# Kernel tuning notes

Hardware: AMD Instinct MI355X
Metric: run time of the kernel (lower is better)

## Reference

```python
import jax, jax.numpy as jnp
import numpy as np

B, H, S, D = 4, 16, 2048, 128


def setup_inputs() -> dict:
    key = jax.random.key(0)
    kq, kk, kv, km = jax.random.split(key, 4)
    query = jax.random.normal(kq, (B, H, S, D), dtype=jnp.float32)
    k = jax.random.normal(kk, (B, H, S, D), dtype=jnp.float32)
    value = jax.random.normal(kv, (B, H, S, D), dtype=jnp.float32)
    mask = jax.random.randint(km, (B, 1, S, S), 0, 2, dtype=jnp.int32)
    return {"query": query, "key": k, "value": value, "mask": mask, "softmax_dim": -1}


def reference(query, key, value, mask, softmax_dim):
    dk = query.shape[-1]
    # scores: [B, H, S, S]
    scores = jnp.einsum("bhqd,bhkd->bhqk", query, key) / jnp.sqrt(jnp.float32(dk))
    scores = jnp.where(mask == 0, jnp.float32(-1e9), scores)
    attention = jax.nn.softmax(scores, axis=softmax_dim)
    out = jnp.einsum("bhqk,bhkd->bhqd", attention, value)
    return (out, attention)
```

## Files before the change

### kernel.cpp

```cpp
#include <hip/hip_runtime.h>

typedef __attribute__((ext_vector_type(8))) short short8;
typedef __attribute__((ext_vector_type(4))) short short4v;
typedef __attribute__((ext_vector_type(4))) float float4v;

#define B_ 4
#define H_ 16
#define S_ 2048
#define D_ 128
#define BM 64
#define NKT64 32
#define NKT32 64

#define NSH (B_ * H_ * S_ * D_)
#define NMW ((size_t)B_ * 32 * S_)
#define WS_NEED (2ull * (unsigned long long)NSH * 2ull + (unsigned long long)NMW * 8ull)

#define QSCALE (0.08838834764831845f * 1.4426950408889634f)

__device__ __forceinline__ unsigned cvtpk(float lo, float hi) {
  unsigned r;
  asm("v_cvt_pk_bf16_f32 %0, %1, %2" : "=v"(r) : "v"(lo), "v"(hi));
  return r;
}

__device__ __forceinline__ short f2bf(float f) {
  unsigned u = __float_as_uint(f);
  u = (u + 0x7fffu + ((u >> 16) & 1u)) >> 16;
  return (short)u;
}

__device__ __forceinline__ void gl16(const void* g, void* lds) {
  __builtin_amdgcn_global_load_lds(
      (const __attribute__((address_space(1))) unsigned int*)g,
      (__attribute__((address_space(3))) unsigned int*)lds, 16, 0, 0);
}

__global__ void prep_kv(const float* __restrict__ Kg, const float* __restrict__ Vg,
                        short* __restrict__ Kf, short* __restrict__ Vf, int half) {
  size_t id = (size_t)blockIdx.x * 256 + threadIdx.x;
  if (blockIdx.x < (unsigned)half) {
    int c  = (int)(id & 15);
    int g  = (int)((id >> 4) & 3);
    int dc = (int)((id >> 6) & 3);
    int kf = (int)((id >> 8) & 3);
    int kt = (int)((id >> 10) & 31);
    size_t bh = id >> 15;
    const float* src = Kg + ((bh * S_ + (size_t)(kt * 64 + kf * 16 + c)) * D_) + dc * 32 + g * 8;
    float4v a = *(const float4v*)src;
    float4v b = *(const float4v*)(src + 4);
    int4 s;
    s.x = (int)cvtpk(a[0], a[1]);
    s.y = (int)cvtpk(a[2], a[3]);
    s.z = (int)cvtpk(b[0], b[1]);
    s.w = (int)cvtpk(b[2], b[3]);
    ((int4*)Kf)[id] = s;
  } else {
    id -= (size_t)half * 256;
    int c   = (int)(id & 15);
    int g   = (int)((id >> 4) & 3);
    int df  = (int)((id >> 6) & 7);
    int kt32= (int)((id >> 9) & 63);
    size_t bh = id >> 15;
    const float* src = Vg + (bh * S_ + (size_t)(kt32 * 32 + g * 8)) * D_ + df * 16 + c;
    float f[8];
#pragma unroll
    for (int e = 0; e < 8; ++e) f[e] = src[(size_t)e * D_];
    int4 s;
    s.x = (int)cvtpk(f[0], f[1]);
    s.y = (int)cvtpk(f[2], f[3]);
    s.z = (int)cvtpk(f[4], f[5]);
    s.w = (int)cvtpk(f[6], f[7]);
    ((int4*)Vf)[id] = s;
  }
}

__global__ void prep_m(const int* __restrict__ Mg, unsigned long long* __restrict__ Bits) {
  int gw = blockIdx.x * 4 + (threadIdx.x >> 6);
  int j  = threadIdx.x & 63;
  int kt = gw & 31;
  int q  = (gw >> 5) & (S_ - 1);
  int b  = gw >> 16;
  int m = Mg[((size_t)b * S_ + q) * S_ + kt * 64 + j];
  unsigned long long bal = __ballot(m != 0);
  if (j == 0) Bits[((size_t)b * 32 + kt) * S_ + q] = bal;
}

__global__ __launch_bounds__(256, 4) void sdpa_main(
    const float* __restrict__ Qg, const short* __restrict__ Kfr,
    const short* __restrict__ Vfr, const unsigned long long* __restrict__ Bits,
    float* __restrict__ Og, float* __restrict__ Ag) {

  __shared__ __align__(16) char smem[32768 + 5120];
  short (*Ps)[40] = (short (*)[40])(smem + 32768);

  const int t = threadIdx.x;
  const int w = t >> 6;
  const int l = t & 63;
  const int g = l >> 4;

  const int p    = blockIdx.x;
  const int xcd  = p & 7;
  const int slot = p >> 3;
  const int grp  = ((slot >> 5) << 3) + xcd;
  const int qt   = slot & 31;
  const int h    = grp & 15;
  const int b    = grp >> 4;

  const int qbase  = qt * BM;
  const int qrow_l = w * 16 + (l & 15);
  const int qrow   = qbase + qrow_l;

  const size_t bhOff = (size_t)(b * H_ + h) * (S_ * D_);
  const short* Kp = Kfr + bhOff;
  const short* Vp = Vfr + bhOff;
  const unsigned long long* Bp = Bits + (size_t)b * 32 * S_;
  const unsigned* Bu = (const unsigned*)Bits;
  float* Op = Og + bhOff;
  float* Ap = Ag + (size_t)(b * H_ + h) * ((size_t)S_ * S_);

  short8 qf[4];
#pragma unroll
  for (int dc = 0; dc < 4; ++dc) {
    const float* qsrc = Qg + bhOff + (size_t)qrow * D_ + dc * 32 + g * 8;
    float4v a = *(const float4v*)qsrc;
    float4v c4 = *(const float4v*)(qsrc + 4);
    int4 s;
    s.x = (int)cvtpk(a[0] * QSCALE, a[1] * QSCALE);
    s.y = (int)cvtpk(a[2] * QSCALE, a[3] * QSCALE);
    s.z = (int)cvtpk(c4[0] * QSCALE, c4[1] * QSCALE);
    s.w = (int)cvtpk(c4[2] * QSCALE, c4[3] * QSCALE);
    qf[dc] = *(short8*)&s;
  }

#pragma unroll
  for (int i = 0; i < 4; ++i) {
    int f = w * 4 + i;
    gl16(Kp + f * 512 + l * 8, smem + f * 1024);
  }
  __syncthreads();

  float ls0 = 0.f, ls1 = 0.f, ls2 = 0.f, ls3 = 0.f;
  unsigned long long mb = Bp[qrow];
  int cur = 0;
  for (int kt = 0; kt < NKT64; ++kt) {
    unsigned long long mb_next = 0;
    if (kt < NKT64 - 1) {
      mb_next = Bp[(size_t)(kt + 1) * S_ + qrow];
      const short* src = Kp + (size_t)(kt + 1) * 8192;
      char* dst = smem + (cur ^ 1) * 16384;
#pragma unroll
      for (int i = 0; i < 4; ++i) {
        int f = w * 4 + i;
        gl16(src + f * 512 + l * 8, dst + f * 1024);
      }
    }
    const char* kb = smem + cur * 16384;

    float4v acc[4];
#pragma unroll
    for (int kf = 0; kf < 4; ++kf) acc[kf] = (float4v){0.f, 0.f, 0.f, 0.f};
#pragma unroll
    for (int kf = 0; kf < 4; ++kf) {
#pragma unroll
      for (int dc = 0; dc < 4; ++dc) {
        short8 af = *(const short8*)(kb + (kf * 4 + dc) * 1024 + l * 16);
        acc[kf] = __builtin_amdgcn_mfma_f32_16x16x32_bf16(af, qf[dc], acc[kf], 0, 0, 0);
      }
    }
#pragma unroll
    for (int kf = 0; kf < 4; ++kf) {
      unsigned mg = (unsigned)(mb >> (kf * 16 + g * 4)) & 0xFu;
      float p0 = ((mg >> 0) & 1) ? __builtin_amdgcn_exp2f(acc[kf][0]) : 0.f;
      float p1 = ((mg >> 1) & 1) ? __builtin_amdgcn_exp2f(acc[kf][1]) : 0.f;
      float p2 = ((mg >> 2) & 1) ? __builtin_amdgcn_exp2f(acc[kf][2]) : 0.f;
      float p3 = ((mg >> 3) & 1) ? __builtin_amdgcn_exp2f(acc[kf][3]) : 0.f;
      if (kf == 0) ls0 += (p0 + p1) + (p2 + p3);
      else if (kf == 1) ls1 += (p0 + p1) + (p2 + p3);
      else if (kf == 2) ls2 += (p0 + p1) + (p2 + p3);
      else ls3 += (p0 + p1) + (p2 + p3);
    }
    __syncthreads();
    mb = mb_next;
    cur ^= 1;
  }
  float lsum = (ls0 + ls1) + (ls2 + ls3);
  lsum += __shfl_xor(lsum, 16);
  lsum += __shfl_xor(lsum, 32);
  const float lg = (lsum > 0.f) ? __log2f(lsum) : 1e30f;

#pragma unroll
  for (int i = 0; i < 2; ++i) {
    int f = w + 4 * i;
    gl16(Kp + f * 512 + l * 8, smem + f * 1024);
    gl16(Vp + f * 512 + l * 8, smem + 16384 + f * 1024);
  }
  __syncthreads();

  float4v acco[8];
#pragma unroll
  for (int df = 0; df < 8; ++df) acco[df] = (float4v){0.f, 0.f, 0.f, 0.f};

  unsigned mw = Bu[((size_t)(b * 32) * S_ + qrow) * 2];
  cur = 0;
  for (int kt = 0; kt < NKT32; ++kt) {
    unsigned mw_next = 0;
    if (kt < NKT32 - 1) {
      mw_next = Bu[((size_t)(b * 32 + ((kt + 1) >> 1)) * S_ + qrow) * 2 + ((kt + 1) & 1)];
      const short* ks = Kp + (size_t)(kt + 1) * 4096;
      const short* vs = Vp + (size_t)(kt + 1) * 4096;
      char* kd = smem + (cur ^ 1) * 8192;
      char* vd = smem + 16384 + (cur ^ 1) * 8192;
#pragma unroll
      for (int i = 0; i < 2; ++i) {
        int f = w + 4 * i;
        gl16(ks + f * 512 + l * 8, kd + f * 1024);
        gl16(vs + f * 512 + l * 8, vd + f * 1024);
      }
    }
    const char* kb = smem + cur * 8192;
    const char* vb = smem + 16384 + cur * 8192;

    float4v acc[2];
#pragma unroll
    for (int kf = 0; kf < 2; ++kf) acc[kf] = (float4v){0.f, 0.f, 0.f, 0.f};
#pragma unroll
    for (int kf = 0; kf < 2; ++kf) {
#pragma unroll
      for (int dc = 0; dc < 4; ++dc) {
        short8 af = *(const short8*)(kb + (kf * 4 + dc) * 1024 + l * 16);
        acc[kf] = __builtin_amdgcn_mfma_f32_16x16x32_bf16(af, qf[dc], acc[kf], 0, 0, 0);
      }
    }

    float4v aw[2];
#pragma unroll
    for (int kf = 0; kf < 2; ++kf) {
      unsigned mg = (mw >> (kf * 16 + g * 4)) & 0xFu;
#pragma unroll
      for (int r = 0; r < 4; ++r) {
        float arg = ((mg >> r) & 1) ? (acc[kf][r] - lg) : -1e30f;
        aw[kf][r] = __builtin_amdgcn_exp2f(arg);
      }
      int2 pb;
      pb.x = (int)cvtpk(aw[kf][0], aw[kf][1]);
      pb.y = (int)cvtpk(aw[kf][2], aw[kf][3]);
      *(int2*)&Ps[qrow_l][kf * 16 + g * 4] = pb;
    }

    {
      short8 pbf = *(const short8*)&Ps[qrow_l][g * 8];
#pragma unroll
      for (int df = 0; df < 8; ++df) {
        short8 vf = *(const short8*)(vb + df * 1024 + l * 16);
        acco[df] = __builtin_amdgcn_mfma_f32_16x16x32_bf16(vf, pbf, acco[df], 0, 0, 0);
      }
    }
#pragma unroll
    for (int kf = 0; kf < 2; ++kf) {
      int k0 = kt * 32 + kf * 16 + g * 4;
      __builtin_nontemporal_store(aw[kf], (float4v*)(Ap + (size_t)qrow * S_ + k0));
    }
    __syncthreads();
    mw = mw_next;
    cur ^= 1;
  }

#pragma unroll
  for (int df = 0; df < 8; ++df) {
    __builtin_nontemporal_store(acco[df], (float4v*)(Op + (size_t)qrow * D_ + df * 16 + g * 4));
  }
}

#define LQK 136
#define LVT 72

__global__ __launch_bounds__(256, 3) void sdpa_fallback(
    const float* __restrict__ Qg, const float* __restrict__ Kg,
    const float* __restrict__ Vg, const int* __restrict__ Mg,
    float* __restrict__ Og, float* __restrict__ Ag) {

  __shared__ __align__(16) char smemf[17408 + 27648];
  short (*Ks)[LQK]  = (short (*)[LQK])(smemf);
  short (*Qs)[LQK]  = (short (*)[LQK])(smemf + 17408);
  short (*VTs)[LVT] = (short (*)[LVT])(smemf + 17408);
  short (*Psf)[LVT] = (short (*)[LVT])(smemf + 17408 + 18432);

  const int t = threadIdx.x;
  const int w = t >> 6;
  const int l = t & 63;
  const int g = l >> 4;
  const int c = l & 15;

  const int bid = blockIdx.x;
  const int qt = bid & 31;
  const int h  = (bid >> 5) & 15;
  const int b  = bid >> 9;

  const int qbase  = qt * BM;
  const int qrow_l = w * 16 + c;
  const int qrow   = qbase + qrow_l;

  const size_t bhOff = (size_t)(b * H_ + h) * (S_ * D_);
  const float* Qp = Qg + bhOff;
  const float* Kp = Kg + bhOff;
  const float* Vp = Vg + bhOff;
  const int*   Mp = Mg + (size_t)b * S_ * S_;
  float* Op = Og + bhOff;
  float* Ap = Ag + (size_t)(b * H_ + h) * ((size_t)S_ * S_);

#pragma unroll
  for (int i = 0; i < 8; ++i) {
    int idx = t + i * 256;
    int d4 = idx & 31, row = idx >> 5;
    float4v v = *(const float4v*)(Qp + (size_t)(qbase + row) * D_ + d4 * 4);
    short4v s;
    s[0] = f2bf(v[0] * QSCALE); s[1] = f2bf(v[1] * QSCALE);
    s[2] = f2bf(v[2] * QSCALE); s[3] = f2bf(v[3] * QSCALE);
    *(short4v*)&Qs[row][d4 * 4] = s;
  }
  __syncthreads();

  short8 qf[4];
#pragma unroll
  for (int dc = 0; dc < 4; ++dc)
    qf[dc] = *(const short8*)&Qs[qrow_l][dc * 32 + g * 8];

  float m_run = -1e30f, l_run = 0.f;
  for (int kt = 0; kt < 32; ++kt) {
    __syncthreads();
#pragma unroll
    for (int i = 0; i < 8; ++i) {
      int idx = t + i * 256;
      int d4 = idx & 31, row = idx >> 5;
      float4v v = *(const float4v*)(Kp + (size_t)(kt * 64 + row) * D_ + d4 * 4);
      short4v s;
      s[0] = f2bf(v[0]); s[1] = f2bf(v[1]); s[2] = f2bf(v[2]); s[3] = f2bf(v[3]);
      *(short4v*)&Ks[row][d4 * 4] = s;
    }
    __syncthreads();

    float4v acc[4];
#pragma unroll
    for (int kf = 0; kf < 4; ++kf) acc[kf] = (float4v){0.f, 0.f, 0.f, 0.f};
#pragma unroll
    for (int kf = 0; kf < 4; ++kf) {
#pragma unroll
      for (int dc = 0; dc < 4; ++dc) {
        short8 af = *(const short8*)&Ks[kf * 16 + c][dc * 32 + g * 8];
        acc[kf] = __builtin_amdgcn_mfma_f32_16x16x32_bf16(af, qf[dc], acc[kf], 0, 0, 0);
      }
    }

    float sv[4][4];
    float tmax = -1e30f;
#pragma unroll
    for (int kf = 0; kf < 4; ++kf) {
      int k0 = kt * 64 + kf * 16 + g * 4;
      const int4 mv = *(const int4*)(Mp + (size_t)qrow * S_ + k0);
      int mr[4] = {mv.x, mv.y, mv.z, mv.w};
#pragma unroll
      for (int r = 0; r < 4; ++r) {
        float x = acc[kf][r];
        x = (mr[r] == 0) ? -1e9f : x;
        sv[kf][r] = x;
        tmax = fmaxf(tmax, x);
      }
    }
    tmax = fmaxf(tmax, __shfl_xor(tmax, 16));
    tmax = fmaxf(tmax, __shfl_xor(tmax, 32));
    float newm = fmaxf(m_run, tmax);
    float tsum = 0.f;
#pragma unroll
    for (int kf = 0; kf < 4; ++kf)
#pragma unroll
      for (int r = 0; r < 4; ++r)
        tsum += __builtin_amdgcn_exp2f(sv[kf][r] - newm);
    tsum += __shfl_xor(tsum, 16);
    tsum += __shfl_xor(tsum, 32);
    l_run = l_run * __builtin_amdgcn_exp2f(m_run - newm) + tsum;
    m_run = newm;
  }

  const float rl = 1.0f / l_run;

  float4v acco[8];
#pragma unroll
  for (int df = 0; df < 8; ++df) acco[df] = (float4v){0.f, 0.f, 0.f, 0.f};

  for (int kt = 0; kt < 32; ++kt) {
    __syncthreads();
#pragma unroll
    for (int i = 0; i < 8; ++i) {
      int idx = t + i * 256;
      int d4 = idx & 31, row = idx >> 5;
      float4v v = *(const float4v*)(Kp + (size_t)(kt * 64 + row) * D_ + d4 * 4);
      short4v s;
      s[0] = f2bf(v[0]); s[1] = f2bf(v[1]); s[2] = f2bf(v[2]); s[3] = f2bf(v[3]);
      *(short4v*)&Ks[row][d4 * 4] = s;
    }
#pragma unroll
    for (int i = 0; i < 8; ++i) {
      int idx = t + i * 256;
      int d = idx & 127, kq = idx >> 7;
      const float* vp = Vp + (size_t)(kt * 64 + kq * 4) * D_ + d;
      short4v s;
      s[0] = f2bf(vp[0]); s[1] = f2bf(vp[D_]); s[2] = f2bf(vp[2 * D_]); s[3] = f2bf(vp[3 * D_]);
      *(short4v*)&VTs[d][kq * 4] = s;
    }
    __syncthreads();

    float4v acc[4];
#pragma unroll
    for (int kf = 0; kf < 4; ++kf) acc[kf] = (float4v){0.f, 0.f, 0.f, 0.f};
#pragma unroll
    for (int kf = 0; kf < 4; ++kf) {
#pragma unroll
      for (int dc = 0; dc < 4; ++dc) {
        short8 af = *(const short8*)&Ks[kf * 16 + c][dc * 32 + g * 8];
        acc[kf] = __builtin_amdgcn_mfma_f32_16x16x32_bf16(af, qf[dc], acc[kf], 0, 0, 0);
      }
    }

#pragma unroll
    for (int kf = 0; kf < 4; ++kf) {
      int k0 = kt * 64 + kf * 16 + g * 4;
      const int4 mv = *(const int4*)(Mp + (size_t)qrow * S_ + k0);
      int mr[4] = {mv.x, mv.y, mv.z, mv.w};
      float4v aw;
      short4v pb;
#pragma unroll
      for (int r = 0; r < 4; ++r) {
        float x = acc[kf][r];
        x = (mr[r] == 0) ? -1e9f : x;
        float pn = __builtin_amdgcn_exp2f(x - m_run) * rl;
        aw[r] = pn;
        pb[r] = f2bf(pn);
      }
      __builtin_nontemporal_store(aw, (float4v*)(Ap + (size_t)qrow * S_ + k0));
      *(short4v*)&Psf[qrow_l][kf * 16 + g * 4] = pb;
    }

#pragma unroll
    for (int kc = 0; kc < 2; ++kc) {
      short8 pbf = *(const short8*)&Psf[qrow_l][kc * 32 + g * 8];
#pragma unroll
      for (int df = 0; df < 8; ++df) {
        short8 vf = *(const short8*)&VTs[df * 16 + c][kc * 32 + g * 8];
        acco[df] = __builtin_amdgcn_mfma_f32_16x16x32_bf16(vf, pbf, acco[df], 0, 0, 0);
      }
    }
  }

#pragma unroll
  for (int df = 0; df < 8; ++df) {
    *(float4v*)(Op + (size_t)qrow * D_ + df * 16 + g * 4) = acco[df];
  }
}

extern "C" void kernel_launch(void* const* d_in, const int* in_sizes, int n_in,
                              void* d_out, int out_size, void* d_ws, size_t ws_size,
                              hipStream_t stream) {
  const float* Q = (const float*)d_in[0];
  const float* K = (const float*)d_in[1];
  const float* V = (const float*)d_in[2];
  const int*   M = (const int*)d_in[3];
  float* Out  = (float*)d_out;
  float* Attn = Out + (size_t)B_ * H_ * S_ * D_;

  if (ws_size >= WS_NEED) {
    short* Kf = (short*)d_ws;
    short* Vf = Kf + (size_t)NSH;
    unsigned long long* Bits = (unsigned long long*)(Vf + (size_t)NSH);
    const int pgrid = NSH / 8 / 256;
    prep_kv<<<dim3(pgrid * 2), dim3(256), 0, stream>>>(K, V, Kf, Vf, pgrid);
    prep_m<<<dim3((unsigned)(NMW / 4)), dim3(256), 0, stream>>>(M, Bits);
    sdpa_main<<<dim3(B_ * H_ * (S_ / BM)), dim3(256), 0, stream>>>(
        Q, Kf, Vf, Bits, Out, Attn);
  } else {
    sdpa_fallback<<<dim3(B_ * H_ * (S_ / BM)), dim3(256), 0, stream>>>(Q, K, V, M, Out, Attn);
  }
}
```

Before: 432.5 us.

## Prefetch K/V tiles two iterations ahead with explicit vmcnt waits

Both main loops now keep two tiles in flight instead of one. They issue loads for tile kt+2 into the freed buffer after the compute barrier, and gate each iteration with hand-counted s_waitcnt vmcnt values plus a raw s_barrier in place of __syncthreads. The aim is to hide global-to-LDS latency and avoid draining all outstanding memory operations, including the attention nontemporal stores, at every barrier. The risk is that the hand-counted vmcnt values are fragile: if the compiler reorders or adds memory operations, a wait may be too loose and read stale LDS.

```diff
diff --git a/kernel.cpp b/kernel.cpp
--- a/kernel.cpp
+++ b/kernel.cpp
@@ -17,6 +17,12 @@
 #define WS_NEED (2ull * (unsigned long long)NSH * 2ull + (unsigned long long)NMW * 8ull)
 
 #define QSCALE (0.08838834764831845f * 1.4426950408889634f)
+
+#define WAITV0() asm volatile("s_waitcnt vmcnt(0)" ::: "memory")
+#define WAITV2() asm volatile("s_waitcnt vmcnt(2)" ::: "memory")
+#define WAITV5() asm volatile("s_waitcnt vmcnt(5)" ::: "memory")
+#define WAITV7() asm volatile("s_waitcnt vmcnt(7)" ::: "memory")
+#define BARR()   asm volatile("s_barrier" ::: "memory")
 
 __device__ __forceinline__ unsigned cvtpk(float lo, float hi) {
   unsigned r;
@@ -138,24 +144,19 @@
     int f = w * 4 + i;
     gl16(Kp + f * 512 + l * 8, smem + f * 1024);
   }
-  __syncthreads();
+  unsigned long long mb0 = Bp[qrow];
+#pragma unroll
+  for (int i = 0; i < 4; ++i) {
+    int f = w * 4 + i;
+    gl16(Kp + 8192 + f * 512 + l * 8, smem + 16384 + f * 1024);
+  }
+  unsigned long long mb1 = Bp[(size_t)S_ + qrow];
 
   float ls0 = 0.f, ls1 = 0.f, ls2 = 0.f, ls3 = 0.f;
-  unsigned long long mb = Bp[qrow];
-  int cur = 0;
   for (int kt = 0; kt < NKT64; ++kt) {
-    unsigned long long mb_next = 0;
-    if (kt < NKT64 - 1) {
-      mb_next = Bp[(size_t)(kt + 1) * S_ + qrow];
-      const short* src = Kp + (size_t)(kt + 1) * 8192;
-      char* dst = smem + (cur ^ 1) * 16384;
-#pragma unroll
-      for (int i = 0; i < 4; ++i) {
-        int f = w * 4 + i;
-        gl16(src + f * 512 + l * 8, dst + f * 1024);
-      }
-    }
-    const char* kb = smem + cur * 16384;
+    if (kt < NKT64 - 1) { WAITV5(); } else { WAITV0(); }
+    BARR();
+    const char* kb = smem + (kt & 1) * 16384;
 
     float4v acc[4];
 #pragma unroll
@@ -170,7 +171,7 @@
     }
 #pragma unroll
     for (int kf = 0; kf < 4; ++kf) {
-      unsigned mg = (unsigned)(mb >> (kf * 16 + g * 4)) & 0xFu;
+      unsigned mg = (unsigned)(mb0 >> (kf * 16 + g * 4)) & 0xFu;
       float p0 = ((mg >> 0) & 1) ? __builtin_amdgcn_exp2f(acc[kf][0]) : 0.f;
       float p1 = ((mg >> 1) & 1) ? __builtin_amdgcn_exp2f(acc[kf][1]) : 0.f;
       float p2 = ((mg >> 2) & 1) ? __builtin_amdgcn_exp2f(acc[kf][2]) : 0.f;
@@ -180,9 +181,19 @@
       else if (kf == 2) ls2 += (p0 + p1) + (p2 + p3);
       else ls3 += (p0 + p1) + (p2 + p3);
     }
-    __syncthreads();
-    mb = mb_next;
-    cur ^= 1;
+    BARR();
+    unsigned long long mb2 = 0;
+    if (kt < NKT64 - 2) {
+      const short* src = Kp + (size_t)(kt + 2) * 8192;
+      char* dst = smem + (kt & 1) * 16384;
+#pragma unroll
+      for (int i = 0; i < 4; ++i) {
+        int f = w * 4 + i;
+        gl16(src + f * 512 + l * 8, dst + f * 1024);
+      }
+      mb2 = Bp[(size_t)(kt + 2) * S_ + qrow];
+    }
+    mb0 = mb1; mb1 = mb2;
   }
   float lsum = (ls0 + ls1) + (ls2 + ls3);
   lsum += __shfl_xor(lsum, 16);
@@ -195,75 +206,83 @@
     gl16(Kp + f * 512 + l * 8, smem + f * 1024);
     gl16(Vp + f * 512 + l * 8, smem + 16384 + f * 1024);
   }
-  __syncthreads();
+  unsigned mw0 = Bu[((size_t)(b * 32) * S_ + qrow) * 2];
+#pragma unroll
+  for (int i = 0; i < 2; ++i) {
+    int f = w + 4 * i;
+    gl16(Kp + 4096 + f * 512 + l * 8, smem + 8192 + f * 1024);
+    gl16(Vp + 4096 + f * 512 + l * 8, smem + 16384 + 8192 + f * 1024);
+  }
+  unsigned mw1 = Bu[((size_t)(b * 32) * S_ + qrow) * 2 + 1];
 
   float4v acco[8];
 #pragma unroll
   for (int df = 0; df < 8; ++df) acco[df] = (float4v){0.f, 0.f, 0.f, 0.f};
 
-  unsigned mw = Bu[((size_t)(b * 32) * S_ + qrow) * 2];
-  cur = 0;
   for (int kt = 0; kt < NKT32; ++kt) {
-    unsigned mw_next = 0;
-    if (kt < NKT32 - 1) {
-      mw_next = Bu[((size_t)(b * 32 + ((kt + 1) >> 1)) * S_ + qrow) * 2 + ((kt + 1) & 1)];
-      const short* ks = Kp + (size_t)(kt + 1) * 4096;
-      const short* vs = Vp + (size_t)(kt + 1) * 4096;
-      char* kd = smem + (cur ^ 1) * 8192;
-      char* vd = smem + 16384 + (cur ^ 1) * 8192;
+    if (kt == 0) { WAITV5(); }
+    else if (kt < NKT32 - 1) { WAITV7(); }
+    else { WAITV2(); }
+    BARR();
+    const char* kb = smem + (kt & 1) * 8192;
+    const char* vb = smem + 16384 + (kt & 1) * 8192;
+
+    float4v acc[2];
+#pragma unroll
+    for (int kf = 0; kf < 2; ++kf) acc[kf] = (float4v){0.f, 0.f, 0.f, 0.f};
+#pragma unroll
+    for (int kf = 0; kf < 2; ++kf) {
+#pragma unroll
+      for (int dc = 0; dc < 4; ++dc) {
+        short8 af = *(const short8*)(kb + (kf * 4 + dc) * 1024 + l * 16);
+        acc[kf] = __builtin_amdgcn_mfma_f32_16x16x32_bf16(af, qf[dc], acc[kf], 0, 0, 0);
+      }
+    }
+
+    float4v aw[2];
+#pragma unroll
+    for (int kf = 0; kf < 2; ++kf) {
+      unsigned mg = (mw0 >> (kf * 16 + g * 4)) & 0xFu;
+#pragma unroll
+      for (int r = 0; r < 4; ++r) {
+        float arg = ((mg >> r) & 1) ? (acc[kf][r] - lg) : -1e30f;
+        aw[kf][r] = __builtin_amdgcn_exp2f(arg);
+      }
+      int2 pb;
+      pb.x = (int)cvtpk(aw[kf][0], aw[kf][1]);
+      pb.y = (int)cvtpk(aw[kf][2], aw[kf][3]);
+      *(int2*)&Ps[qrow_l][kf * 16 + g * 4] = pb;
+    }
+
+    {
+      short8 pbf = *(const short8*)&Ps[qrow_l][g * 8];
+#pragma unroll
+      for (int df = 0; df < 8; ++df) {
+        short8 vf = *(const short8*)(vb + df * 1024 + l * 16);
+        acco[df] = __builtin_amdgcn_mfma_f32_16x16x32_bf16(vf, pbf, acco[df], 0, 0, 0);
+      }
+    }
+    BARR();
+    unsigned mw2 = 0;
+    if (kt < NKT32 - 2) {
+      const short* ks = Kp + (size_t)(kt + 2) * 4096;
+      const short* vs = Vp + (size_t)(kt + 2) * 4096;
+      char* kd = smem + (kt & 1) * 8192;
+      char* vd = smem + 16384 + (kt & 1) * 8192;
 #pragma unroll
       for (int i = 0; i < 2; ++i) {
         int f = w + 4 * i;
         gl16(ks + f * 512 + l * 8, kd + f * 1024);
         gl16(vs + f * 512 + l * 8, vd + f * 1024);
       }
-    }
-    const char* kb = smem + cur * 8192;
-    const char* vb = smem + 16384 + cur * 8192;
-
-    float4v acc[2];
-#pragma unroll
-    for (int kf = 0; kf < 2; ++kf) acc[kf] = (float4v){0.f, 0.f, 0.f, 0.f};
-#pragma unroll
-    for (int kf = 0; kf < 2; ++kf) {
-#pragma unroll
-      for (int dc = 0; dc < 4; ++dc) {
-        short8 af = *(const short8*)(kb + (kf * 4 + dc) * 1024 + l * 16);
-        acc[kf] = __builtin_amdgcn_mfma_f32_16x16x32_bf16(af, qf[dc], acc[kf], 0, 0, 0);
-      }
-    }
-
-    float4v aw[2];
-#pragma unroll
-    for (int kf = 0; kf < 2; ++kf) {
-      unsigned mg = (mw >> (kf * 16 + g * 4)) & 0xFu;
-#pragma unroll
-      for (int r = 0; r < 4; ++r) {
-        float arg = ((mg >> r) & 1) ? (acc[kf][r] - lg) : -1e30f;
-        aw[kf][r] = __builtin_amdgcn_exp2f(arg);
-      }
-      int2 pb;
-      pb.x = (int)cvtpk(aw[kf][0], aw[kf][1]);
-      pb.y = (int)cvtpk(aw[kf][2], aw[kf][3]);
-      *(int2*)&Ps[qrow_l][kf * 16 + g * 4] = pb;
-    }
-
-    {
-      short8 pbf = *(const short8*)&Ps[qrow_l][g * 8];
-#pragma unroll
-      for (int df = 0; df < 8; ++df) {
-        short8 vf = *(const short8*)(vb + df * 1024 + l * 16);
-        acco[df] = __builtin_amdgcn_mfma_f32_16x16x32_bf16(vf, pbf, acco[df], 0, 0, 0);
-      }
+      mw2 = Bu[((size_t)(b * 32 + ((kt + 2) >> 1)) * S_ + qrow) * 2 + ((kt + 2) & 1)];
     }
 #pragma unroll
     for (int kf = 0; kf < 2; ++kf) {
       int k0 = kt * 32 + kf * 16 + g * 4;
       __builtin_nontemporal_store(aw[kf], (float4v*)(Ap + (size_t)qrow * S_ + k0));
     }
-    __syncthreads();
-    mw = mw_next;
-    cur ^= 1;
+    mw0 = mw1; mw1 = mw2;
   }
 
 #pragma unroll
```

New measurement: 437.8 us. No clear change (+1.2%).

## Double query tile per block so each wave reuses K/V fragments across two row groups

Applied to the files above, without the earlier changes.

Raises the query tile from 64 to 128 rows, with each wave handling two 16-row groups that share every K and V fragment loaded from LDS. This halves K/V global and LDS traffic per query row and halves the block count. In exchange it doubles accumulator registers, lowers the occupancy hint from 4 to 3 blocks, grows shared memory for P, and leaves fewer blocks to fill the GPU. The fallback kernel is pinned to the old 64-row tiling.

```diff
diff --git a/kernel.cpp b/kernel.cpp
--- a/kernel.cpp
+++ b/kernel.cpp
@@ -8,7 +8,7 @@
 #define H_ 16
 #define S_ 2048
 #define D_ 128
-#define BM 64
+#define BM 128
 #define NKT64 32
 #define NKT32 64
 
@@ -86,12 +86,12 @@
   if (j == 0) Bits[((size_t)b * 32 + kt) * S_ + q] = bal;
 }
 
-__global__ __launch_bounds__(256, 4) void sdpa_main(
+__global__ __launch_bounds__(256, 3) void sdpa_main(
     const float* __restrict__ Qg, const short* __restrict__ Kfr,
     const short* __restrict__ Vfr, const unsigned long long* __restrict__ Bits,
     float* __restrict__ Og, float* __restrict__ Ag) {
 
-  __shared__ __align__(16) char smem[32768 + 5120];
+  __shared__ __align__(16) char smem[32768 + 10240];
   short (*Ps)[40] = (short (*)[40])(smem + 32768);
 
   const int t = threadIdx.x;
@@ -102,14 +102,15 @@
   const int p    = blockIdx.x;
   const int xcd  = p & 7;
   const int slot = p >> 3;
-  const int grp  = ((slot >> 5) << 3) + xcd;
-  const int qt   = slot & 31;
+  const int grp  = ((slot >> 4) << 3) + xcd;
+  const int qt   = slot & 15;
   const int h    = grp & 15;
   const int b    = grp >> 4;
 
   const int qbase  = qt * BM;
-  const int qrow_l = w * 16 + (l & 15);
-  const int qrow   = qbase + qrow_l;
+  const int r0     = w * 32 + (l & 15);
+  const int qrow0  = qbase + r0;
+  const int qrow1  = qrow0 + 16;
 
   const size_t bhOff = (size_t)(b * H_ + h) * (S_ * D_);
   const short* Kp = Kfr + bhOff;
@@ -119,18 +120,26 @@
   float* Op = Og + bhOff;
   float* Ap = Ag + (size_t)(b * H_ + h) * ((size_t)S_ * S_);
 
-  short8 qf[4];
+  short8 qf0[4], qf1[4];
 #pragma unroll
   for (int dc = 0; dc < 4; ++dc) {
-    const float* qsrc = Qg + bhOff + (size_t)qrow * D_ + dc * 32 + g * 8;
-    float4v a = *(const float4v*)qsrc;
-    float4v c4 = *(const float4v*)(qsrc + 4);
+    const float* q0 = Qg + bhOff + (size_t)qrow0 * D_ + dc * 32 + g * 8;
+    float4v a = *(const float4v*)q0;
+    float4v c4 = *(const float4v*)(q0 + 4);
     int4 s;
     s.x = (int)cvtpk(a[0] * QSCALE, a[1] * QSCALE);
     s.y = (int)cvtpk(a[2] * QSCALE, a[3] * QSCALE);
     s.z = (int)cvtpk(c4[0] * QSCALE, c4[1] * QSCALE);
     s.w = (int)cvtpk(c4[2] * QSCALE, c4[3] * QSCALE);
-    qf[dc] = *(short8*)&s;
+    qf0[dc] = *(short8*)&s;
+    const float* q1 = Qg + bhOff + (size_t)qrow1 * D_ + dc * 32 + g * 8;
+    a = *(const float4v*)q1;
+    c4 = *(const float4v*)(q1 + 4);
+    s.x = (int)cvtpk(a[0] * QSCALE, a[1] * QSCALE);
+    s.y = (int)cvtpk(a[2] * QSCALE, a[3] * QSCALE);
+    s.z = (int)cvtpk(c4[0] * QSCALE, c4[1] * QSCALE);
+    s.w = (int)cvtpk(c4[2] * QSCALE, c4[3] * QSCALE);
+    qf1[dc] = *(short8*)&s;
   }
 
 #pragma unroll
@@ -140,13 +149,14 @@
   }
   __syncthreads();
 
-  float ls0 = 0.f, ls1 = 0.f, ls2 = 0.f, ls3 = 0.f;
-  unsigned long long mb = Bp[qrow];
+  float lsA0 = 0.f, lsA1 = 0.f, lsB0 = 0.f, lsB1 = 0.f;
+  unsigned long long mbA = Bp[qrow0], mbB = Bp[qrow1];
   int cur = 0;
   for (int kt = 0; kt < NKT64; ++kt) {
-    unsigned long long mb_next = 0;
+    unsigned long long mbA2 = 0, mbB2 = 0;
     if (kt < NKT64 - 1) {
-      mb_next = Bp[(size_t)(kt + 1) * S_ + qrow];
+      mbA2 = Bp[(size_t)(kt + 1) * S_ + qrow0];
+      mbB2 = Bp[(size_t)(kt + 1) * S_ + qrow1];
       const short* src = Kp + (size_t)(kt + 1) * 8192;
       char* dst = smem + (cur ^ 1) * 16384;
 #pragma unroll
@@ -157,37 +167,45 @@
     }
     const char* kb = smem + cur * 16384;
 
-    float4v acc[4];
-#pragma unroll
-    for (int kf = 0; kf < 4; ++kf) acc[kf] = (float4v){0.f, 0.f, 0.f, 0.f};
+    float4v accA[4], accB[4];
+#pragma unroll
+    for (int kf = 0; kf < 4; ++kf) { accA[kf] = (float4v){0.f,0.f,0.f,0.f}; accB[kf] = (float4v){0.f,0.f,0.f,0.f}; }
 #pragma unroll
     for (int kf = 0; kf < 4; ++kf) {
 #pragma unroll
       for (int dc = 0; dc < 4; ++dc) {
         short8 af = *(const short8*)(kb + (kf * 4 + dc) * 1024 + l * 16);
-        acc[kf] = __builtin_amdgcn_mfma_f32_16x16x32_bf16(af, qf[dc], acc[kf], 0, 0, 0);
+        accA[kf] = __builtin_amdgcn_mfma_f32_16x16x32_bf16(af, qf0[dc], accA[kf], 0, 0, 0);
+        accB[kf] = __builtin_amdgcn_mfma_f32_16x16x32_bf16(af, qf1[dc], accB[kf], 0, 0, 0);
       }
     }
 #pragma unroll
     for (int kf = 0; kf < 4; ++kf) {
-      unsigned mg = (unsigned)(mb >> (kf * 16 + g * 4)) & 0xFu;
-      float p0 = ((mg >> 0) & 1) ? __builtin_amdgcn_exp2f(acc[kf][0]) : 0.f;
-      float p1 = ((mg >> 1) & 1) ? __builtin_amdgcn_exp2f(acc[kf][1]) : 0.f;
-      float p2 = ((mg >> 2) & 1) ? __builtin_amdgcn_exp2f(acc[kf][2]) : 0.f;
-      float p3 = ((mg >> 3) & 1) ? __builtin_amdgcn_exp2f(acc[kf][3]) : 0.f;
-      if (kf == 0) ls0 += (p0 + p1) + (p2 + p3);
-      else if (kf == 1) ls1 += (p0 + p1) + (p2 + p3);
-      else if (kf == 2) ls2 += (p0 + p1) + (p2 + p3);
-      else ls3 += (p0 + p1) + (p2 + p3);
+      unsigned mgA = (unsigned)(mbA >> (kf * 16 + g * 4)) & 0xFu;
+      float a0 = ((mgA >> 0) & 1) ? __builtin_amdgcn_exp2f(accA[kf][0]) : 0.f;
+      float a1 = ((mgA >> 1) & 1) ? __builtin_amdgcn_exp2f(accA[kf][1]) : 0.f;
+      float a2 = ((mgA >> 2) & 1) ? __builtin_amdgcn_exp2f(accA[kf][2]) : 0.f;
+      float a3 = ((mgA >> 3) & 1) ? __builtin_amdgcn_exp2f(accA[kf][3]) : 0.f;
+      if (kf & 1) lsA1 += (a0 + a1) + (a2 + a3); else lsA0 += (a0 + a1) + (a2 + a3);
+      unsigned mgB = (unsigned)(mbB >> (kf * 16 + g * 4)) & 0xFu;
+      float b0 = ((mgB >> 0) & 1) ? __builtin_amdgcn_exp2f(accB[kf][0]) : 0.f;
+      float b1 = ((mgB >> 1) & 1) ? __builtin_amdgcn_exp2f(accB[kf][1]) : 0.f;
+      float b2 = ((mgB >> 2) & 1) ? __builtin_amdgcn_exp2f(accB[kf][2]) : 0.f;
+      float b3 = ((mgB >> 3) & 1) ? __builtin_amdgcn_exp2f(accB[kf][3]) : 0.f;
+      if (kf & 1) lsB1 += (b0 + b1) + (b2 + b3); else lsB0 += (b0 + b1) + (b2 + b3);
     }
     __syncthreads();
-    mb = mb_next;
+    mbA = mbA2; mbB = mbB2;
     cur ^= 1;
   }
-  float lsum = (ls0 + ls1) + (ls2 + ls3);
-  lsum += __shfl_xor(lsum, 16);
-  lsum += __shfl_xor(lsum, 32);
-  const float lg = (lsum > 0.f) ? __log2f(lsum) : 1e30f;
+  float lsumA = lsA0 + lsA1;
+  lsumA += __shfl_xor(lsumA, 16);
+  lsumA += __shfl_xor(lsumA, 32);
+  const float lgA = (lsumA > 0.f) ? __log2f(lsumA) : 1e30f;
+  float lsumB = lsB0 + lsB1;
+  lsumB += __shfl_xor(lsumB, 16);
+  lsumB += __shfl_xor(lsumB, 32);
+  const float lgB = (lsumB > 0.f) ? __log2f(lsumB) : 1e30f;
 
 #pragma unroll
   for (int i = 0; i < 2; ++i) {
@@ -197,16 +215,18 @@
   }
   __syncthreads();
 
-  float4v acco[8];
-#pragma unroll
-  for (int df = 0; df < 8; ++df) acco[df] = (float4v){0.f, 0.f, 0.f, 0.f};
-
-  unsigned mw = Bu[((size_t)(b * 32) * S_ + qrow) * 2];
+  float4v accoA[8], accoB[8];
+#pragma unroll
+  for (int df = 0; df < 8; ++df) { accoA[df] = (float4v){0.f,0.f,0.f,0.f}; accoB[df] = (float4v){0.f,0.f,0.f,0.f}; }
+
+  unsigned mwA = Bu[((size_t)(b * 32) * S_ + qrow0) * 2];
+  unsigned mwB = Bu[((size_t)(b * 32) * S_ + qrow1) * 2];
   cur = 0;
   for (int kt = 0; kt < NKT32; ++kt) {
-    unsigned mw_next = 0;
+    unsigned mwA2 = 0, mwB2 = 0;
     if (kt < NKT32 - 1) {
-      mw_next = Bu[((size_t)(b * 32 + ((kt + 1) >> 1)) * S_ + qrow) * 2 + ((kt + 1) & 1)];
+      mwA2 = Bu[((size_t)(b * 32 + ((kt + 1) >> 1)) * S_ + qrow0) * 2 + ((kt + 1) & 1)];
+      mwB2 = Bu[((size_t)(b * 32 + ((kt + 1) >> 1)) * S_ + qrow1) * 2 + ((kt + 1) & 1)];
       const short* ks = Kp + (size_t)(kt + 1) * 4096;
       const short* vs = Vp + (size_t)(kt + 1) * 4096;
       char* kd = smem + (cur ^ 1) * 8192;
@@ -221,54 +241,68 @@
     const char* kb = smem + cur * 8192;
     const char* vb = smem + 16384 + cur * 8192;
 
-    float4v acc[2];
-#pragma unroll
-    for (int kf = 0; kf < 2; ++kf) acc[kf] = (float4v){0.f, 0.f, 0.f, 0.f};
+    float4v accA[2], accB[2];
+#pragma unroll
+    for (int kf = 0; kf < 2; ++kf) { accA[kf] = (float4v){0.f,0.f,0.f,0.f}; accB[kf] = (float4v){0.f,0.f,0.f,0.f}; }
 #pragma unroll
     for (int kf = 0; kf < 2; ++kf) {
 #pragma unroll
       for (int dc = 0; dc < 4; ++dc) {
         short8 af = *(const short8*)(kb + (kf * 4 + dc) * 1024 + l * 16);
-        acc[kf] = __builtin_amdgcn_mfma_f32_16x16x32_bf16(af, qf[dc], acc[kf], 0, 0, 0);
-      }
-    }
-
-    float4v aw[2];
+        accA[kf] = __builtin_amdgcn_mfma_f32_16x16x32_bf16(af, qf0[dc], accA[kf], 0, 0, 0);
+        accB[kf] = __builtin_amdgcn_mfma_f32_16x16x32_bf16(af, qf1[dc], accB[kf], 0, 0, 0);
+      }
+    }
+
+    float4v awA[2], awB[2];
 #pragma unroll
     for (int kf = 0; kf < 2; ++kf) {
-      unsigned mg = (mw >> (kf * 16 + g * 4)) & 0xFu;
+      unsigned mgA = (mwA >> (kf * 16 + g * 4)) & 0xFu;
 #pragma unroll
       for (int r = 0; r < 4; ++r) {
-        float arg = ((mg >> r) & 1) ? (acc[kf][r] - lg) : -1e30f;
-        aw[kf][r] = __builtin_amdgcn_exp2f(arg);
+        float arg = ((mgA >> r) & 1) ? (accA[kf][r] - lgA) : -1e30f;
+        awA[kf][r] = __builtin_amdgcn_exp2f(arg);
       }
       int2 pb;
-      pb.x = (int)cvtpk(aw[kf][0], aw[kf][1]);
-      pb.y = (int)cvtpk(aw[kf][2], aw[kf][3]);
-      *(int2*)&Ps[qrow_l][kf * 16 + g * 4] = pb;
+      pb.x = (int)cvtpk(awA[kf][0], awA[kf][1]);
+      pb.y = (int)cvtpk(awA[kf][2], awA[kf][3]);
+      *(int2*)&Ps[r0][kf * 16 + g * 4] = pb;
+      unsigned mgB = (mwB >> (kf * 16 + g * 4)) & 0xFu;
+#pragma unroll
+      for (int r = 0; r < 4; ++r) {
+        float arg = ((mgB >> r) & 1) ? (accB[kf][r] - lgB) : -1e30f;
+        awB[kf][r] = __builtin_amdgcn_exp2f(arg);
+      }
+      pb.x = (int)cvtpk(awB[kf][0], awB[kf][1]);
+      pb.y = (int)cvtpk(awB[kf][2], awB[kf][3]);
+      *(int2*)&Ps[r0 + 16][kf * 16 + g * 4] = pb;
     }
 
     {
-      short8 pbf = *(const short8*)&Ps[qrow_l][g * 8];
+      short8 pbfA = *(const short8*)&Ps[r0][g * 8];
+      short8 pbfB = *(const short8*)&Ps[r0 + 16][g * 8];
 #pragma unroll
       for (int df = 0; df < 8; ++df) {
         short8 vf = *(const short8*)(vb + df * 1024 + l * 16);
-        acco[df] = __builtin_amdgcn_mfma_f32_16x16x32_bf16(vf, pbf, acco[df], 0, 0, 0);
+        accoA[df] = __builtin_amdgcn_mfma_f32_16x16x32_bf16(vf, pbfA, accoA[df], 0, 0, 0);
+        accoB[df] = __builtin_amdgcn_mfma_f32_16x16x32_bf16(vf, pbfB, accoB[df], 0, 0, 0);
       }
     }
 #pragma unroll
     for (int kf = 0; kf < 2; ++kf) {
       int k0 = kt * 32 + kf * 16 + g * 4;
-      __builtin_nontemporal_store(aw[kf], (float4v*)(Ap + (size_t)qrow * S_ + k0));
+      __builtin_nontemporal_store(awA[kf], (float4v*)(Ap + (size_t)qrow0 * S_ + k0));
+      __builtin_nontemporal_store(awB[kf], (float4v*)(Ap + (size_t)qrow1 * S_ + k0));
     }
     __syncthreads();
-    mw = mw_next;
+    mwA = mwA2; mwB = mwB2;
     cur ^= 1;
   }
 
 #pragma unroll
   for (int df = 0; df < 8; ++df) {
-    __builtin_nontemporal_store(acco[df], (float4v*)(Op + (size_t)qrow * D_ + df * 16 + g * 4));
+    __builtin_nontemporal_store(accoA[df], (float4v*)(Op + (size_t)qrow0 * D_ + df * 16 + g * 4));
+    __builtin_nontemporal_store(accoB[df], (float4v*)(Op + (size_t)qrow1 * D_ + df * 16 + g * 4));
   }
 }
 
@@ -297,7 +331,7 @@
   const int h  = (bid >> 5) & 15;
   const int b  = bid >> 9;
 
-  const int qbase  = qt * BM;
+  const int qbase  = qt * 64;
   const int qrow_l = w * 16 + c;
   const int qrow   = qbase + qrow_l;
 
@@ -478,6 +512,6 @@
     sdpa_main<<<dim3(B_ * H_ * (S_ / BM)), dim3(256), 0, stream>>>(
         Q, Kf, Vf, Bits, Out, Attn);
   } else {
-    sdpa_fallback<<<dim3(B_ * H_ * (S_ / BM)), dim3(256), 0, stream>>>(Q, K, V, M, Out, Attn);
-  }
-}
+    sdpa_fallback<<<dim3(B_ * H_ * 32), dim3(256), 0, stream>>>(Q, K, V, M, Out, Attn);
+  }
+}
```

After: 496.1 us. +14.7%, slower.
